# Optimization experiments

Hardware: AMD Instinct MI355X
Metric: run time of the kernel (lower is better)

Reference implementation:

```python
import jax, jax.numpy as jnp
import numpy as np

PIXELS_PER_CELL = (8, 8)
CELLS_PER_BLOCK = (2, 2)
ORIENTATIONS = 9
GRAY_W = jnp.array([0.2125, 0.7154, 0.0721], dtype=jnp.float32)  # skimage rgb2gray
EPS = 1e-5  # skimage L2-Hys eps


def setup_inputs() -> dict:
    key = jax.random.key(0)
    x = jax.random.uniform(key, (64, 512, 512, 3), dtype=jnp.float32)
    return {"x": x}


def _hog(x):
    # rgb2gray
    gray = jnp.einsum("bhwc,c->bhw", x, GRAY_W)  # [B,H,W]
    B, H, W = gray.shape
    pr, pc = PIXELS_PER_CELL
    br, bc = CELLS_PER_BLOCK
    O = ORIENTATIONS

    # skimage _hog_channel_gradient: central differences, zero at borders
    g_row = jnp.zeros_like(gray).at[:, 1:-1, :].set(gray[:, 2:, :] - gray[:, :-2, :])
    g_col = jnp.zeros_like(gray).at[:, :, 1:-1].set(gray[:, :, 2:] - gray[:, :, :-2])

    mag = jnp.hypot(g_row, g_col)
    ori = jnp.rad2deg(jnp.arctan2(g_row, g_col)) % 180.0  # unsigned orientation

    ncr, ncc = H // pr, W // pc
    mag = mag[:, : ncr * pr, : ncc * pc]
    ori = ori[:, : ncr * pr, : ncc * pc]

    spacing = 180.0 / O
    cell_area = float(pr * pc)
    # per-orientation-bin cell histograms: hard binning (skimage cell_hog)
    hists = []
    for o in range(O):
        lo, hi = spacing * o, spacing * (o + 1)
        contrib = jnp.where((ori >= lo) & (ori < hi), mag, 0.0)
        # sum over each pr x pc cell, divide by cell area
        h = contrib.reshape(B, ncr, pr, ncc, pc).sum(axis=(2, 4)) / cell_area
        hists.append(h)
    hist = jnp.stack(hists, axis=-1)  # [B, ncr, ncc, O]

    # overlapping blocks of cells, stride 1 cell
    nbr, nbc = ncr - br + 1, ncc - bc + 1
    block = jnp.stack(
        [jnp.stack([hist[:, r : r + nbr, c : c + nbc, :] for c in range(bc)], axis=3)
         for r in range(br)], axis=3)  # [B, nbr, nbc, br, bc, O]

    # L2-Hys normalization (skimage default block_norm)
    norm = jnp.sqrt(jnp.sum(block * block, axis=(3, 4, 5), keepdims=True) + EPS ** 2)
    blk = jnp.minimum(block / norm, 0.2)
    norm2 = jnp.sqrt(jnp.sum(blk * blk, axis=(3, 4, 5), keepdims=True) + EPS ** 2)
    blk = blk / norm2

    return blk.reshape(B, -1).astype(jnp.float32)


def reference(x):
    return _hog(x)
```

## Files before the change

### kernel.cpp

```cpp
#include <hip/hip_runtime.h>
#include <math.h>

#define IMG_H 512
#define IMG_W 512
#define NCELL 64
#define NORI 9

__device__ __noinline__ float fdlibm_atanf(float x) {
#pragma clang fp contract(off)
    const float atanhi[4] = {4.6364760399e-01f, 7.8539812565e-01f,
                             9.8279368877e-01f, 1.5707962513e+00f};
    const float atanlo[4] = {5.0121582440e-09f, 3.7748947079e-08f,
                             3.4473217170e-08f, 7.5497894159e-08f};
    const float aT[11] = {
        3.3333334327e-01f, -2.0000000298e-01f, 1.4285714924e-01f,
       -1.1111110449e-01f,  9.0908870101e-02f, -7.6918758452e-02f,
        6.6610731184e-02f, -5.8335702866e-02f,  4.9768779427e-02f,
       -3.6531571299e-02f,  1.6285819933e-02f};
    const float one = 1.0f;

    int hx = __float_as_int(x);
    int ix = hx & 0x7fffffff;
    int id;
    if (ix >= 0x4c800000) {
        if (hx > 0) return atanhi[3] + atanlo[3];
        else        return -atanhi[3] - atanlo[3];
    }
    if (ix < 0x3ee00000) {
        if (ix < 0x39800000) {
            return x;
        }
        id = -1;
    } else {
        x = fabsf(x);
        if (ix < 0x3f980000) {
            if (ix < 0x3f300000) { id = 0; x = (2.0f * x - one) / (2.0f + x); }
            else                 { id = 1; x = (x - one) / (x + one); }
        } else {
            if (ix < 0x401c0000) { id = 2; x = (x - 1.5f) / (one + 1.5f * x); }
            else                 { id = 3; x = -1.0f / x; }
        }
    }
    float z = x * x;
    float w = z * z;
    float s1 = z * (aT[0] + w * (aT[2] + w * (aT[4] + w * (aT[6] + w * (aT[8] + w * aT[10])))));
    float s2 = w * (aT[1] + w * (aT[3] + w * (aT[5] + w * (aT[7] + w * aT[9]))));
    if (id < 0) return x - x * (s1 + s2);
    z = atanhi[id] - ((x * (s1 + s2) - atanlo[id]) - x);
    return (hx < 0) ? -z : z;
}

__device__ __noinline__ int fdlibm_bin(float y, float x) {
#pragma clang fp contract(off)
    const float tiny   = 1.0e-30f;
    const float pi_o_2 = 1.5707963705e+00f;
    const float pi     = 3.1415927410e+00f;
    const float pi_lo  = -8.7422776573e-08f;

    int hx = __float_as_int(x), ix = hx & 0x7fffffff;
    int hy = __float_as_int(y), iy = hy & 0x7fffffff;
    float th;
    if (hx == 0x3f800000) { th = fdlibm_atanf(y); }
    else {
        int m = ((hy >> 31) & 1) | ((hx >> 30) & 2);
        if (iy == 0) {
            switch (m) {
                case 0:
                case 1: th = y; break;
                case 2: th =  pi + tiny; break;
                default: th = -pi - tiny; break;
            }
        } else if (ix == 0) {
            th = (hy < 0) ? -pi_o_2 - tiny : pi_o_2 + tiny;
        } else {
            int k = (iy - ix) >> 23;
            float z;
            int mm = m;
            if (k > 26) {
                z = pi_o_2 + 0.5f * pi_lo;
                mm &= 1;
            } else if (k < -26 && hx < 0) {
                z = 0.0f;
            } else {
                z = fdlibm_atanf(fabsf(y / x));
            }
            switch (mm) {
                case 0:  th = z; break;
                case 1:  th = -z; break;
                case 2:  th = pi - (z - pi_lo); break;
                default: th = (z - pi_lo) - pi; break;
            }
        }
    }
    const float RAD2DEG = (float)(180.0 / 3.14159265358979311600e+00);
    float m = fmodf(th * RAD2DEG, 180.0f);
    if (m < 0.0f) m += 180.0f;
    int o = (int)(m * 0.05f);
    if (o < 9) {
        if (m < 20.0f * (float)o) --o;
        else if (m >= 20.0f * (float)(o + 1)) ++o;
    }
    return o;
}

__global__ __launch_bounds__(256) void hog_hist_kernel(const float* __restrict__ x,
                                                       float* __restrict__ hist) {
#pragma clang fp contract(off)
    const int bid = blockIdx.x;
    const int b   = bid >> 6;
    const int cr  = bid & 63;
    const int t   = threadIdx.x;
    const int h0  = cr * 8;

    __shared__ __align__(16) float g[10][IMG_W];
    __shared__ float cellHist[NCELL * NORI];

    for (int i = t; i < NCELL * NORI; i += 256) cellHist[i] = 0.0f;

    const float GW0 = 0.2125f, GW1 = 0.7154f, GW2 = 0.0721f;
    for (int gi = t; gi < 10 * 128; gi += 256) {
        const int rr = gi >> 7;
        int h = h0 - 1 + rr;
        if (h < 0)      h = 1;
        if (h > 511)    h = 510;
        const int grp = gi & 127;
        const float4* p4 = (const float4*)x + (size_t)(b * IMG_H + h) * (IMG_W * 3 / 4)
                           + (size_t)grp * 3;
        float4 a = p4[0], c = p4[1], d = p4[2];
        const int wg = grp * 4;
        g[rr][wg + 0] = __builtin_fmaf(a.z, GW2, __builtin_fmaf(a.y, GW1, a.x * GW0));
        g[rr][wg + 1] = __builtin_fmaf(c.y, GW2, __builtin_fmaf(c.x, GW1, a.w * GW0));
        g[rr][wg + 2] = __builtin_fmaf(d.x, GW2, __builtin_fmaf(c.w, GW1, c.z * GW0));
        g[rr][wg + 3] = __builtin_fmaf(d.w, GW2, __builtin_fmaf(d.z, GW1, d.y * GW0));
    }
    __syncthreads();

    const float PIF   = 3.14159265358979323846f;
    const float PIO2F = 1.57079632679489662f;
    const float PIO4F = 0.78539816339744831f;
    for (int pass = 0; pass < 2; ++pass) {
        const int w  = t + pass * 256;
        const int wl = (w == 0)   ? 0   : w - 1;
        const int wr = (w == 511) ? 511 : w + 1;
        const bool wok = (w >= 1) && (w <= 510);
        const int cellBase = (w >> 3) * NORI;

        float cc[10], ee[8], ww[8];
#pragma unroll
        for (int i = 0; i < 10; ++i) cc[i] = g[i][w];
#pragma unroll
        for (int i = 0; i < 8; ++i) { ee[i] = g[i + 1][wr]; ww[i] = g[i + 1][wl]; }

#pragma unroll
        for (int r = 0; r < 8; ++r) {
            const float gr = cc[r + 2] - cc[r];
            const float gc = wok ? (ee[r] - ww[r]) : 0.0f;
            const float mag = __builtin_amdgcn_sqrtf(__builtin_fmaf(gr, gr, gc * gc));

            const float ax = fabsf(gc), ay = fabsf(gr);
            const float mx = fmaxf(ax, ay), mn = fminf(ax, ay);
            const bool red = mn > 0.4142135624f * mx;
            const float num = red ? (mn - mx) : mn;
            const float den = red ? (mn + mx) : mx;
            const float xx  = num * __builtin_amdgcn_rcpf(den);
            const float z   = xx * xx;
            float y = __builtin_fmaf(
                        __builtin_fmaf(
                          __builtin_fmaf(8.05374449538e-2f, z, -1.38776856032e-1f),
                          z, 1.99777106478e-1f),
                        z, -3.33329491539e-1f);
            float r0 = __builtin_fmaf(y * z, xx, xx);
            if (red)        r0 = PIO4F + r0;
            if (ay > ax)    r0 = PIO2F - r0;
            if (gc < 0.0f)  r0 = PIF - r0;
            if (gr < 0.0f)  r0 = PIF - r0;
            const float q    = (r0 * 57.295779513082323f) * 0.05f;
            int o            = (int)q;
            const float frac = q - (float)o;
            if (frac < 1e-4f || frac > 0.9999f || o > 8) {
                o = fdlibm_bin(gr, gc);
                if (o < 0 || o > 8) continue;
            }
            atomicAdd(&cellHist[cellBase + o], mag);
        }
    }
    __syncthreads();

    float* hout = hist + (size_t)(b * NCELL + cr) * (NCELL * NORI);
    for (int i = t; i < NCELL * NORI; i += 256) hout[i] = cellHist[i] * 0.015625f;
}

__global__ __launch_bounds__(256) void hog_norm_kernel(const float* __restrict__ hist,
                                                       float* __restrict__ out) {
#pragma clang fp contract(off)
    const int bid = blockIdx.x;
    const int b   = bid / 63;
    const int r   = bid % 63;
    const int t   = threadIdx.x;

    __shared__ __align__(16) float hrow[2 * NCELL * NORI];
    __shared__ __align__(16) float orow[63 * 36];

    const float4* src = (const float4*)(hist + (size_t)(b * NCELL + r) * (NCELL * NORI));
    float4* dst = (float4*)hrow;
    for (int i = t; i < 288; i += 256) dst[i] = src[i];
    __syncthreads();

    const int c = t >> 2;
    const int l = t & 3;
    if (c < 63) {
        const int bi = l >> 1, bj = l & 1;
        const float* v = &hrow[(bi * NCELL + (c + bj)) * NORI];
        float vv[9];
        float ss = 0.0f;
#pragma unroll
        for (int k = 0; k < 9; ++k) { vv[k] = v[k]; ss += vv[k] * vv[k]; }
        ss += __shfl_xor(ss, 1, 64);
        ss += __shfl_xor(ss, 2, 64);
        const float n1 = sqrtf(ss + 1e-10f);
        float ss2 = 0.0f;
#pragma unroll
        for (int k = 0; k < 9; ++k) { vv[k] = fminf(vv[k] / n1, 0.2f); ss2 += vv[k] * vv[k]; }
        ss2 += __shfl_xor(ss2, 1, 64);
        ss2 += __shfl_xor(ss2, 2, 64);
        const float n2 = sqrtf(ss2 + 1e-10f);
        float* od = &orow[c * 36 + l * 9];
#pragma unroll
        for (int k = 0; k < 9; ++k) od[k] = vv[k] / n2;
    }
    __syncthreads();

    float4* og = (float4*)(out + (size_t)bid * (63 * 36));
    const float4* os = (const float4*)orow;
    for (int i = t; i < 567; i += 256) og[i] = os[i];
}

extern "C" void kernel_launch(void* const* d_in, const int* in_sizes, int n_in,
                              void* d_out, int out_size, void* d_ws, size_t ws_size,
                              hipStream_t stream) {
    const float* x = (const float*)d_in[0];
    float* out     = (float*)d_out;
    float* hist    = (float*)d_ws;

    hog_hist_kernel<<<dim3(64 * 64), dim3(256), 0, stream>>>(x, hist);
    hog_norm_kernel<<<dim3(64 * 63), dim3(256), 0, stream>>>(hist, out);
}
```

Before: 336.6 us.

## Replace shared-memory atomic histograms with register bins and deferred slow-path queue

The histogram kernel now accumulates each column's 8 pixels into 9 per-thread register bins, reduces across the 8 lanes of a cell with shuffles, and writes cell histograms directly to global memory instead of using shared-memory atomics. Near-boundary orientations are pushed to a small shared queue and resolved afterwards with the exact fdlibm path, so the divergent slow call no longer sits inside the main loop. If the queue overflows, a full recompute pass falls back to global atomics. Input loads are batched into registers before the gray conversion to raise memory-level parallelism. The norm kernel drops shared staging, reads global directly, and multiplies by a reciprocal instead of dividing, which may change rounding slightly.

```diff
diff --git a/kernel.cpp b/kernel.cpp
--- a/kernel.cpp
+++ b/kernel.cpp
@@ -5,6 +5,7 @@
 #define IMG_W 512
 #define NCELL 64
 #define NORI 9
+#define QMAX 128
 
 __device__ __noinline__ float fdlibm_atanf(float x) {
 #pragma clang fp contract(off)
@@ -103,6 +104,39 @@
     return o;
 }
 
+__device__ __forceinline__ void fast_bin(float gr, float gc,
+                                         float& mag, int& o, bool& suspect) {
+#pragma clang fp contract(off)
+    const float PIF   = 3.14159265358979323846f;
+    const float PIO2F = 1.57079632679489662f;
+    const float PIO4F = 0.78539816339744831f;
+
+    mag = __builtin_amdgcn_sqrtf(__builtin_fmaf(gr, gr, gc * gc));
+
+    const float ax = fabsf(gc), ay = fabsf(gr);
+    const float mx = fmaxf(ax, ay), mn = fminf(ax, ay);
+    const bool red = mn > 0.4142135624f * mx;
+    const float num = red ? (mn - mx) : mn;
+    const float den = red ? (mn + mx) : mx;
+    const float xx  = num * __builtin_amdgcn_rcpf(den);
+    const float z   = xx * xx;
+    float y = __builtin_fmaf(
+                __builtin_fmaf(
+                  __builtin_fmaf(8.05374449538e-2f, z, -1.38776856032e-1f),
+                  z, 1.99777106478e-1f),
+                z, -3.33329491539e-1f);
+    float r0 = __builtin_fmaf(y * z, xx, xx);
+    if (red)        r0 = PIO4F + r0;
+    if (ay > ax)    r0 = PIO2F - r0;
+    if (gc < 0.0f)  r0 = PIF - r0;
+    if (gr < 0.0f)  r0 = PIF - r0;
+    const float q    = (r0 * 57.295779513082323f) * 0.05f;
+    o = (int)q;
+    const float frac = q - (float)o;
+    suspect = (frac < 1e-4f) || (frac > 0.9999f) || (o > 8);
+    if (ay == 0.0f) { o = 0; suspect = false; }
+}
+
 __global__ __launch_bounds__(256) void hog_hist_kernel(const float* __restrict__ x,
                                                        float* __restrict__ hist) {
 #pragma clang fp contract(off)
@@ -113,81 +147,115 @@
     const int h0  = cr * 8;
 
     __shared__ __align__(16) float g[10][IMG_W];
-    __shared__ float cellHist[NCELL * NORI];
-
-    for (int i = t; i < NCELL * NORI; i += 256) cellHist[i] = 0.0f;
+    __shared__ float qgr[QMAX], qgc[QMAX], qmag[QMAX];
+    __shared__ int   qcell[QMAX];
+    __shared__ int   nslow;
+
+    if (t == 0) nslow = 0;
 
     const float GW0 = 0.2125f, GW1 = 0.7154f, GW2 = 0.0721f;
-    for (int gi = t; gi < 10 * 128; gi += 256) {
+    float4 A[5], C[5], D[5];
+#pragma unroll
+    for (int k = 0; k < 5; ++k) {
+        const int gi = t + 256 * k;
         const int rr = gi >> 7;
         int h = h0 - 1 + rr;
-        if (h < 0)      h = 1;
-        if (h > 511)    h = 510;
+        if (h < 0)   h = 1;
+        if (h > 511) h = 510;
         const int grp = gi & 127;
         const float4* p4 = (const float4*)x + (size_t)(b * IMG_H + h) * (IMG_W * 3 / 4)
                            + (size_t)grp * 3;
-        float4 a = p4[0], c = p4[1], d = p4[2];
-        const int wg = grp * 4;
-        g[rr][wg + 0] = __builtin_fmaf(a.z, GW2, __builtin_fmaf(a.y, GW1, a.x * GW0));
-        g[rr][wg + 1] = __builtin_fmaf(c.y, GW2, __builtin_fmaf(c.x, GW1, a.w * GW0));
-        g[rr][wg + 2] = __builtin_fmaf(d.x, GW2, __builtin_fmaf(c.w, GW1, c.z * GW0));
-        g[rr][wg + 3] = __builtin_fmaf(d.w, GW2, __builtin_fmaf(d.z, GW1, d.y * GW0));
+        A[k] = p4[0]; C[k] = p4[1]; D[k] = p4[2];
+    }
+#pragma unroll
+    for (int k = 0; k < 5; ++k) {
+        const int gi = t + 256 * k;
+        const int rr = gi >> 7;
+        const int wg = (gi & 127) * 4;
+        g[rr][wg + 0] = __builtin_fmaf(A[k].z, GW2, __builtin_fmaf(A[k].y, GW1, A[k].x * GW0));
+        g[rr][wg + 1] = __builtin_fmaf(C[k].y, GW2, __builtin_fmaf(C[k].x, GW1, A[k].w * GW0));
+        g[rr][wg + 2] = __builtin_fmaf(D[k].x, GW2, __builtin_fmaf(C[k].w, GW1, C[k].z * GW0));
+        g[rr][wg + 3] = __builtin_fmaf(D[k].w, GW2, __builtin_fmaf(D[k].z, GW1, D[k].y * GW0));
     }
     __syncthreads();
 
-    const float PIF   = 3.14159265358979323846f;
-    const float PIO2F = 1.57079632679489662f;
-    const float PIO4F = 0.78539816339744831f;
+    float* hout = hist + (size_t)(b * NCELL + cr) * (NCELL * NORI);
+
     for (int pass = 0; pass < 2; ++pass) {
         const int w  = t + pass * 256;
         const int wl = (w == 0)   ? 0   : w - 1;
         const int wr = (w == 511) ? 511 : w + 1;
         const bool wok = (w >= 1) && (w <= 510);
-        const int cellBase = (w >> 3) * NORI;
+        const int c  = w >> 3;
 
         float cc[10], ee[8], ww[8];
 #pragma unroll
         for (int i = 0; i < 10; ++i) cc[i] = g[i][w];
 #pragma unroll
         for (int i = 0; i < 8; ++i) { ee[i] = g[i + 1][wr]; ww[i] = g[i + 1][wl]; }
+
+        float bh[9];
+#pragma unroll
+        for (int k = 0; k < 9; ++k) bh[k] = 0.0f;
 
 #pragma unroll
         for (int r = 0; r < 8; ++r) {
             const float gr = cc[r + 2] - cc[r];
             const float gc = wok ? (ee[r] - ww[r]) : 0.0f;
-            const float mag = __builtin_amdgcn_sqrtf(__builtin_fmaf(gr, gr, gc * gc));
-
-            const float ax = fabsf(gc), ay = fabsf(gr);
-            const float mx = fmaxf(ax, ay), mn = fminf(ax, ay);
-            const bool red = mn > 0.4142135624f * mx;
-            const float num = red ? (mn - mx) : mn;
-            const float den = red ? (mn + mx) : mx;
-            const float xx  = num * __builtin_amdgcn_rcpf(den);
-            const float z   = xx * xx;
-            float y = __builtin_fmaf(
-                        __builtin_fmaf(
-                          __builtin_fmaf(8.05374449538e-2f, z, -1.38776856032e-1f),
-                          z, 1.99777106478e-1f),
-                        z, -3.33329491539e-1f);
-            float r0 = __builtin_fmaf(y * z, xx, xx);
-            if (red)        r0 = PIO4F + r0;
-            if (ay > ax)    r0 = PIO2F - r0;
-            if (gc < 0.0f)  r0 = PIF - r0;
-            if (gr < 0.0f)  r0 = PIF - r0;
-            const float q    = (r0 * 57.295779513082323f) * 0.05f;
-            int o            = (int)q;
-            const float frac = q - (float)o;
-            if (frac < 1e-4f || frac > 0.9999f || o > 8) {
-                o = fdlibm_bin(gr, gc);
-                if (o < 0 || o > 8) continue;
-            }
-            atomicAdd(&cellHist[cellBase + o], mag);
-        }
-    }
+            float mag; int o; bool suspect;
+            fast_bin(gr, gc, mag, o, suspect);
+            if (suspect) {
+                const int qi = atomicAdd(&nslow, 1);
+                if (qi < QMAX) { qgr[qi] = gr; qgc[qi] = gc; qmag[qi] = mag; qcell[qi] = c; }
+            } else {
+#pragma unroll
+                for (int k = 0; k < 9; ++k) bh[k] += (o == k) ? mag : 0.0f;
+            }
+        }
+
+#pragma unroll
+        for (int k = 0; k < 9; ++k) {
+            bh[k] += __shfl_xor(bh[k], 1, 64);
+            bh[k] += __shfl_xor(bh[k], 2, 64);
+            bh[k] += __shfl_xor(bh[k], 4, 64);
+        }
+        const int j = t & 7;
+        float mv = bh[0];
+#pragma unroll
+        for (int k = 1; k < 8; ++k) mv = (j == k) ? bh[k] : mv;
+        hout[c * NORI + j] = mv * 0.015625f;
+        if (j == 0) hout[c * NORI + 8] = bh[8] * 0.015625f;
+    }
+
     __syncthreads();
 
-    float* hout = hist + (size_t)(b * NCELL + cr) * (NCELL * NORI);
-    for (int i = t; i < NCELL * NORI; i += 256) hout[i] = cellHist[i] * 0.015625f;
+    const int ns = nslow;
+    if (ns <= QMAX) {
+        if (t < ns) {
+            const int o = fdlibm_bin(qgr[t], qgc[t]);
+            if (o >= 0 && o <= 8)
+                atomicAdd(&hout[qcell[t] * NORI + o], qmag[t] * 0.015625f);
+        }
+    } else {
+        for (int pass = 0; pass < 2; ++pass) {
+            const int w  = t + pass * 256;
+            const int wl = (w == 0)   ? 0   : w - 1;
+            const int wr = (w == 511) ? 511 : w + 1;
+            const bool wok = (w >= 1) && (w <= 510);
+            const int c  = w >> 3;
+            for (int r = 0; r < 8; ++r) {
+                const float gr = g[r + 2][w] - g[r][w];
+                const float gc = wok ? (g[r + 1][wr] - g[r + 1][wl]) : 0.0f;
+                float mag; int o; bool suspect;
+                fast_bin(gr, gc, mag, o, suspect);
+                if (suspect) {
+                    const int oo = fdlibm_bin(gr, gc);
+                    if (oo >= 0 && oo <= 8)
+                        atomicAdd(&hout[c * NORI + oo], mag * 0.015625f);
+                }
+            }
+        }
+    }
 }
 
 __global__ __launch_bounds__(256) void hog_norm_kernel(const float* __restrict__ hist,
@@ -197,42 +265,30 @@
     const int b   = bid / 63;
     const int r   = bid % 63;
     const int t   = threadIdx.x;
-
-    __shared__ __align__(16) float hrow[2 * NCELL * NORI];
-    __shared__ __align__(16) float orow[63 * 36];
-
-    const float4* src = (const float4*)(hist + (size_t)(b * NCELL + r) * (NCELL * NORI));
-    float4* dst = (float4*)hrow;
-    for (int i = t; i < 288; i += 256) dst[i] = src[i];
-    __syncthreads();
-
-    const int c = t >> 2;
-    const int l = t & 3;
-    if (c < 63) {
-        const int bi = l >> 1, bj = l & 1;
-        const float* v = &hrow[(bi * NCELL + (c + bj)) * NORI];
-        float vv[9];
-        float ss = 0.0f;
-#pragma unroll
-        for (int k = 0; k < 9; ++k) { vv[k] = v[k]; ss += vv[k] * vv[k]; }
-        ss += __shfl_xor(ss, 1, 64);
-        ss += __shfl_xor(ss, 2, 64);
-        const float n1 = sqrtf(ss + 1e-10f);
-        float ss2 = 0.0f;
-#pragma unroll
-        for (int k = 0; k < 9; ++k) { vv[k] = fminf(vv[k] / n1, 0.2f); ss2 += vv[k] * vv[k]; }
-        ss2 += __shfl_xor(ss2, 1, 64);
-        ss2 += __shfl_xor(ss2, 2, 64);
-        const float n2 = sqrtf(ss2 + 1e-10f);
-        float* od = &orow[c * 36 + l * 9];
-#pragma unroll
-        for (int k = 0; k < 9; ++k) od[k] = vv[k] / n2;
-    }
-    __syncthreads();
-
-    float4* og = (float4*)(out + (size_t)bid * (63 * 36));
-    const float4* os = (const float4*)orow;
-    for (int i = t; i < 567; i += 256) og[i] = os[i];
+    const int c   = t >> 2;
+    const int l   = t & 3;
+    if (c >= 63) return;
+
+    const int bi = l >> 1, bj = l & 1;
+    const float* v = hist + ((size_t)(b * NCELL + r + bi) * NCELL + (c + bj)) * NORI;
+
+    float vv[9];
+    float ss = 0.0f;
+#pragma unroll
+    for (int k = 0; k < 9; ++k) { vv[k] = v[k]; ss += vv[k] * vv[k]; }
+    ss += __shfl_xor(ss, 1, 64);
+    ss += __shfl_xor(ss, 2, 64);
+    const float rn1 = 1.0f / sqrtf(ss + 1e-10f);
+    float ss2 = 0.0f;
+#pragma unroll
+    for (int k = 0; k < 9; ++k) { vv[k] = fminf(vv[k] * rn1, 0.2f); ss2 += vv[k] * vv[k]; }
+    ss2 += __shfl_xor(ss2, 1, 64);
+    ss2 += __shfl_xor(ss2, 2, 64);
+    const float rn2 = 1.0f / sqrtf(ss2 + 1e-10f);
+
+    float* od = out + (size_t)bid * (63 * 36) + (c * 36 + l * 9);
+#pragma unroll
+    for (int k = 0; k < 9; ++k) od[k] = vv[k] * rn2;
 }
 
 extern "C" void kernel_launch(void* const* d_in, const int* in_sizes, int n_in,
```

Measured after the change: 299.3 us. 11.1% less time.
